# Performance work log

Hardware: AMD Instinct MI355X
Metric: run time of the kernel (lower is better)

The kernel has to match this reference:

```python
import jax, jax.numpy as jnp
import numpy as np

B, CIN, COUT, H, W = 2, 64, 64, 64, 2048
EPS = 1e-5


def unfold3(x):
    # x: [B, C, H, W] -> [B, H*W, 9, C], torch.nn.Unfold(k=3, pad=1) layout
    b, c, h, w = x.shape
    xp = jnp.pad(x, ((0, 0), (0, 0), (1, 1), (1, 1)))
    # kernel positions in row-major (ki, kj) order; index 4 is the center
    patches = jnp.stack([xp[:, :, i:i + h, j:j + w]
                         for i in range(3) for j in range(3)], axis=2)  # [B,C,9,H,W]
    return patches.reshape(b, c, 9, h * w).transpose(0, 3, 2, 1)  # [B,HW,9,C]


def setup_inputs() -> dict:
    key = jax.random.key(0)
    ks = jax.random.split(key, 8)
    x = jax.random.normal(ks[0], (B, 3 + CIN, H, W), dtype=jnp.float32)
    mask = jax.random.randint(ks[1], (B, 1, H, W), 0, 2, dtype=jnp.int32)
    w_spatial = jax.random.normal(ks[2], (CIN, 4), dtype=jnp.float32) * 0.5
    b_spatial = jax.random.normal(ks[3], (CIN,), dtype=jnp.float32) * 0.1
    w_channel = jax.random.normal(ks[4], (CIN, 4), dtype=jnp.float32) * 0.5
    b_channel = jax.random.normal(ks[5], (CIN,), dtype=jnp.float32) * 0.1
    w_agg = jax.random.normal(ks[6], (COUT, 9 * CIN), dtype=jnp.float32) * (1.0 / np.sqrt(9 * CIN))
    gamma = jnp.ones((COUT,), dtype=jnp.float32)
    beta = jnp.zeros((COUT,), dtype=jnp.float32)
    return {"x": x, "mask": mask, "w_spatial": w_spatial, "b_spatial": b_spatial,
            "w_channel": w_channel, "b_channel": b_channel, "w_agg": w_agg,
            "gamma": gamma, "beta": beta}


def reference(x, mask, w_spatial, b_spatial, w_channel, b_channel, w_agg, gamma, beta):
    b, _, h, w = x.shape
    x_un = unfold3(x)                              # [B,HW,9,3+C]
    feat = x_un[..., 3:]                           # [B,HW,9,C]
    x_pn = x_un[..., :3]                           # [B,HW,9,3]
    m_un = unfold3(mask.astype(jnp.float32))       # [B,HW,9,1]

    rng = jnp.linalg.norm(x_pn, axis=-1, keepdims=True)
    x_pn4 = jnp.concatenate([x_pn, rng], axis=-1)  # [B,HW,9,4]
    pn_p0 = x_pn4 - x_pn4[:, :, 4:5, :]            # relative to 3x3 center

    ws = jnp.einsum('bnkm,cm->bnkc', pn_p0, w_spatial) + b_spatial
    wc = jnp.einsum('bnkm,cm->bnkc', pn_p0, w_channel) + b_channel
    ws = jnp.max(ws, axis=3, keepdims=True)        # [B,HW,9,1]
    wc = jnp.max(wc, axis=2, keepdims=True)        # [B,HW,1,C]
    ws = jax.nn.softmax(ws, axis=2)
    wc = jax.nn.softmax(wc, axis=3)
    weights = (ws + wc) * m_un                     # [B,HW,9,C]

    feat = (weights * feat).reshape(b, h * w, 9 * CIN)
    out = jnp.einsum('bnf,of->bno', feat, w_agg)   # [B,HW,COUT]
    out = out.transpose(0, 2, 1)                   # [B,COUT,HW]

    # BatchNorm1d in training mode: stats over (batch, spatial) per channel
    mu = jnp.mean(out, axis=(0, 2), keepdims=True)
    var = jnp.mean((out - mu) ** 2, axis=(0, 2), keepdims=True)
    out = (out - mu) * jax.lax.rsqrt(var + EPS)
    out = out * gamma[None, :, None] + beta[None, :, None]
    out = jax.nn.relu(out)
    return out.reshape(b, COUT, h, w)              # Fold(k=1) == reshape
```

## Files before the change

### kernel.cpp

```cpp
#include <hip/hip_runtime.h>
#include <hip/hip_bf16.h>
#include <math.h>
#include <cstddef>

#define HDIM 64
#define WDIM 2048
#define HW   (HDIM*WDIM)
#define BATCH 2
#define CIN  64
#define COUT 64
#define XC   (3+CIN)
#define NPIX (BATCH*HW)
#define NBLK (NPIX/64)
#define NB2  (NBLK*2)
#define EPS  1e-5f

typedef short  short8  __attribute__((ext_vector_type(8)));
typedef float  f32x16  __attribute__((ext_vector_type(16)));

__device__ __forceinline__ unsigned short f2bf(float f) {
    unsigned int u = __float_as_uint(f);
    u += 0x7fff + ((u >> 16) & 1);
    return (unsigned short)(u >> 16);
}

struct __align__(16) SmemA {
    float wsm[9][64];
    float wcpart[4][64];
    float wcsum[4][64];
    float wc[64][64];
    union {
        unsigned short V[2][64][72];
        float wspart[9][4][64];
    } u;
};

__global__ __launch_bounds__(256)
void kernelW(const float* __restrict__ w_agg, unsigned short* __restrict__ wbf)
{
    int t = blockIdx.x*256 + threadIdx.x;
    int co  = t / 72;
    int rem = t % 72;
    int kk  = rem >> 3;
    int ks  = (rem >> 1) & 3;
    int half= rem & 1;
    const float* src = w_agg + (size_t)co*576 + kk*64 + ks*16 + half*8;
    unsigned long long pk0 = 0, pk1 = 0;
    #pragma unroll
    for (int j=0;j<4;++j) pk0 |= (unsigned long long)f2bf(src[j])   << (16*j);
    #pragma unroll
    for (int j=0;j<4;++j) pk1 |= (unsigned long long)f2bf(src[4+j]) << (16*j);
    unsigned long long* dst =
        (unsigned long long*)(wbf + ((size_t)(((kk*4+ks)*2+half)*64 + co))*8);
    dst[0] = pk0; dst[1] = pk1;
}

__global__ __launch_bounds__(256, 4)
void kernelA(const float* __restrict__ x, const int* __restrict__ mask,
             const float* __restrict__ w_sp, const float* __restrict__ b_sp,
             const float* __restrict__ w_ch, const float* __restrict__ b_ch,
             const unsigned short* __restrict__ wbf,
             float* __restrict__ out, float* __restrict__ psum, float* __restrict__ psq)
{
    __shared__ SmemA s;
    const int tid = threadIdx.x;
    const int bid = blockIdx.x;
    const int b  = bid >> 11;
    const int r  = bid & 2047;
    const int h  = r >> 5;
    const int w0 = (r & 31) << 6;

    const int px = tid & 63;
    const int q  = tid >> 6;

    float p[9][4];
    float mkr[9];
    {
        const int wpix = w0 + px;
        #pragma unroll
        for (int k = 0; k < 9; ++k) {
            int hh = h + k/3 - 1;
            int ww = wpix + k%3 - 1;
            bool in = (hh >= 0) && (hh < HDIM) && (ww >= 0) && (ww < WDIM);
            float p0=0.f, p1=0.f, p2=0.f, mv=0.f;
            if (in) {
                size_t base = ((size_t)(b*XC)*HDIM + hh)*(size_t)WDIM + ww;
                p0 = x[base];
                p1 = x[base + (size_t)HW];
                p2 = x[base + 2*(size_t)HW];
                mv = (float)mask[((size_t)b*HDIM + hh)*(size_t)WDIM + ww];
            }
            p[k][0]=p0; p[k][1]=p1; p[k][2]=p2;
            p[k][3]=sqrtf(p0*p0 + p1*p1 + p2*p2);
            mkr[k]=mv;
        }
        float c0=p[4][0], c1=p[4][1], c2=p[4][2], c3=p[4][3];
        #pragma unroll
        for (int k = 0; k < 9; ++k) {
            p[k][0]-=c0; p[k][1]-=c1; p[k][2]-=c2; p[k][3]-=c3;
        }
    }

    float wsp[9];
    #pragma unroll
    for (int k=0;k<9;++k) wsp[k] = -1e30f;
    float tmaxv[16];
    float cqm = -1e30f;
    for (int cc = 0; cc < 16; ++cc) {
        int c = q*16 + cc;
        float a0=w_sp[c*4+0], a1=w_sp[c*4+1], a2=w_sp[c*4+2], a3=w_sp[c*4+3], bs=b_sp[c];
        float d0=w_ch[c*4+0], d1=w_ch[c*4+1], d2=w_ch[c*4+2], d3=w_ch[c*4+3], bc=b_ch[c];
        float tmax = bc;
        wsp[4] = fmaxf(wsp[4], bs);
        #pragma unroll
        for (int k=0;k<9;++k) {
            if (k == 4) continue;
            float sv = fmaf(p[k][0],a0, fmaf(p[k][1],a1, fmaf(p[k][2],a2, fmaf(p[k][3],a3, bs))));
            wsp[k] = fmaxf(wsp[k], sv);
            float tv = fmaf(p[k][0],d0, fmaf(p[k][1],d1, fmaf(p[k][2],d2, fmaf(p[k][3],d3, bc))));
            tmax = fmaxf(tmax, tv);
        }
        tmaxv[cc] = tmax;
        cqm = fmaxf(cqm, tmax);
    }
    #pragma unroll
    for (int k=0;k<9;++k) s.u.wspart[k][q][px] = wsp[k];
    s.wcpart[q][px] = cqm;
    __syncthreads();

    {
        float mxc = fmaxf(fmaxf(s.wcpart[0][px], s.wcpart[1][px]),
                          fmaxf(s.wcpart[2][px], s.wcpart[3][px]));
        float sum = 0.f;
        #pragma unroll
        for (int cc=0; cc<16; ++cc) {
            float e = __expf(tmaxv[cc] - mxc);
            s.wc[q*16+cc][px] = e;
            sum += e;
        }
        s.wcsum[q][px] = sum;
    }
    if (q == 0) {
        float v[9]; float mx = -1e30f;
        #pragma unroll
        for (int k=0;k<9;++k) {
            float a = s.u.wspart[k][0][px];
            a = fmaxf(a, s.u.wspart[k][1][px]);
            a = fmaxf(a, s.u.wspart[k][2][px]);
            a = fmaxf(a, s.u.wspart[k][3][px]);
            v[k]=a; mx=fmaxf(mx,a);
        }
        float sum=0.f;
        #pragma unroll
        for (int k=0;k<9;++k) { v[k]=__expf(v[k]-mx); sum+=v[k]; }
        float inv = 1.0f/sum;
        #pragma unroll
        for (int k=0;k<9;++k) s.wsm[k][px] = v[k]*inv*mkr[k];
    }
    __syncthreads();

    const float winv = 1.0f / (s.wcsum[0][px] + s.wcsum[1][px] +
                               s.wcsum[2][px] + s.wcsum[3][px]);

    const int lane = tid & 63;
    const int wv   = tid >> 6;
    const int mrow = lane & 31;
    const int half = lane >> 5;
    const int co0  = (wv & 1) * 32;
    const int px0  = (wv >> 1) * 32;

    const short8* aswz = (const short8*)wbf;

    f32x16 acc;
    #pragma unroll
    for (int i=0;i<16;++i) acc[i]=0.f;

    auto stage_load = [&](int kk, float* f) {
        int di = kk/3 - 1, dj = (kk%3) - 1;
        int hh = h + di;
        int ww = w0 + px + dj;
        bool inb = (hh>=0) && (hh<HDIM) && (ww>=0) && (ww<WDIM);
        int hhc = hh<0?0:(hh>HDIM-1?HDIM-1:hh);
        int wwc = ww<0?0:(ww>WDIM-1?WDIM-1:ww);
        const float* xb = x + ((size_t)(b*XC + 3)*HDIM + hhc)*(size_t)WDIM + wwc;
        #pragma unroll
        for (int j=0;j<16;++j)
            f[j] = inb ? xb[(size_t)(16*q + j)*HW] : 0.f;
    };
    auto stage_write = [&](int kk, const float* f, int buf) {
        float a_k = s.wsm[kk][px];
        float m2  = mkr[kk] * winv;
        unsigned int packed[8];
        #pragma unroll
        for (int j=0;j<8;++j) {
            unsigned c0 = 16u*q + 2u*j;
            float w0f = fmaf(m2, s.wc[c0][px],   a_k) * f[2*j];
            float w1f = fmaf(m2, s.wc[c0+1][px], a_k) * f[2*j+1];
            __hip_bfloat162 h2 = __float22bfloat162_rn(float2{w0f, w1f});
            unsigned int u; __builtin_memcpy(&u, &h2, 4);
            packed[j] = u;
        }
        uint4* vp = (uint4*)&s.u.V[buf][px][16*q];
        vp[0] = uint4{packed[0],packed[1],packed[2],packed[3]};
        vp[1] = uint4{packed[4],packed[5],packed[6],packed[7]};
    };

    {
        float f0[16];
        stage_load(0, f0);
        stage_write(0, f0, 0);
        __syncthreads();
    }

    for (int kk = 0; kk < 9; ++kk) {
        short8 afc[4];
        #pragma unroll
        for (int ks=0; ks<4; ++ks)
            afc[ks] = aswz[(size_t)(((kk*4+ks)*2+half)*64) + co0 + mrow];

        float fn[16];
        if (kk < 8) stage_load(kk+1, fn);

        const unsigned short* Vb = &s.u.V[kk & 1][px0 + mrow][0];
        #pragma unroll
        for (int ks=0; ks<4; ++ks) {
            short8 bf = *(const short8*)&Vb[ks*16 + half*8];
            acc = __builtin_amdgcn_mfma_f32_32x32x16_bf16(afc[ks], bf, acc, 0, 0, 0);
        }

        if (kk < 8) {
            stage_write(kk+1, fn, (kk & 1) ^ 1);
            __syncthreads();
        }
    }

    const int pxg = w0 + px0 + mrow;
    #pragma unroll
    for (int reg=0; reg<16; ++reg) {
        int row = (reg&3) + 8*(reg>>2) + 4*half;
        int co  = co0 + row;
        float v = acc[reg];
        out[((size_t)(b*COUT+co))*HW + (size_t)h*WDIM + pxg] = v;
        float s1 = v, s2 = v*v;
        #pragma unroll
        for (int m=1; m<32; m<<=1) {
            s1 += __shfl_xor(s1, m, 64);
            s2 += __shfl_xor(s2, m, 64);
        }
        if (mrow == 0) {
            psum[(size_t)co*NB2 + bid*2 + (wv>>1)] = s1;
            psq [(size_t)co*NB2 + bid*2 + (wv>>1)] = s2;
        }
    }
}

__global__ __launch_bounds__(256)
void kernelB(const float* __restrict__ psum, const float* __restrict__ psq,
             float* __restrict__ stats)
{
    int co = blockIdx.x;
    int tid = threadIdx.x;
    float s=0.f, sq=0.f;
    for (int j = tid; j < NB2; j += 256) {
        s  += psum[(size_t)co*NB2 + j];
        sq += psq [(size_t)co*NB2 + j];
    }
    #pragma unroll
    for (int m=1; m<64; m<<=1) { s += __shfl_xor(s,m,64); sq += __shfl_xor(sq,m,64); }
    __shared__ float rs[4], rq[4];
    int wv = tid>>6;
    if ((tid&63)==0){ rs[wv]=s; rq[wv]=sq; }
    __syncthreads();
    if (tid==0) {
        float S = rs[0]+rs[1]+rs[2]+rs[3];
        float Q = rq[0]+rq[1]+rq[2]+rq[3];
        float mu = S / (float)NPIX;
        float var = Q/(float)NPIX - mu*mu;
        stats[co]      = mu;
        stats[64+co]   = rsqrtf(var + EPS);
    }
}

__global__ __launch_bounds__(256)
void kernelC(float* __restrict__ out, const float* __restrict__ stats,
             const float* __restrict__ gamma, const float* __restrict__ beta)
{
    size_t idx8 = (size_t)blockIdx.x*256 + threadIdx.x;
    size_t flat = idx8*8;
    int co = (int)((flat >> 17) & 63);
    float mu = stats[co], rstd = stats[64+co];
    float g  = gamma[co]*rstd;
    float bb = fmaf(-mu, g, beta[co]);
    #pragma unroll
    for (int t=0;t<2;++t) {
        float4 v = *(float4*)(out + flat + t*4);
        v.x = fmaxf(fmaf(v.x, g, bb), 0.f);
        v.y = fmaxf(fmaf(v.y, g, bb), 0.f);
        v.z = fmaxf(fmaf(v.z, g, bb), 0.f);
        v.w = fmaxf(fmaf(v.w, g, bb), 0.f);
        *(float4*)(out + flat + t*4) = v;
    }
}

extern "C" void kernel_launch(void* const* d_in, const int* in_sizes, int n_in,
                              void* d_out, int out_size, void* d_ws, size_t ws_size,
                              hipStream_t stream)
{
    const float* x     = (const float*)d_in[0];
    const int*   mask  = (const int*)  d_in[1];
    const float* w_sp  = (const float*)d_in[2];
    const float* b_sp  = (const float*)d_in[3];
    const float* w_ch  = (const float*)d_in[4];
    const float* b_ch  = (const float*)d_in[5];
    const float* w_agg = (const float*)d_in[6];
    const float* gamma = (const float*)d_in[7];
    const float* beta  = (const float*)d_in[8];
    float* out  = (float*)d_out;
    float* psum = (float*)d_ws;
    float* psq  = psum + (size_t)COUT*NB2;
    float* stats= psq  + (size_t)COUT*NB2;
    unsigned short* wbf = (unsigned short*)(stats + 128);

    kernelW<<<18, 256, 0, stream>>>(w_agg, wbf);
    kernelA<<<NBLK, 256, 0, stream>>>(x, mask, w_sp, b_sp, w_ch, b_ch, wbf, out, psum, psq);
    kernelB<<<COUT, 256, 0, stream>>>(psum, psq, stats);
    int grid_c = (NPIX*COUT/8)/256;
    kernelC<<<grid_c, 256, 0, stream>>>(out, stats, gamma, beta);
}
```

Measured before the change: 290.3 us.

## Stage 3-row halo feature tile in LDS once and build weighted operand in registers

Instead of reloading all 64 channels from global memory for each of the 9 kernel offsets, the block loads a 3x66 halo tile of bf16 features into swizzled LDS once. The per-channel softmax exponentials are also stored as bf16 in LDS, with per-quarter max rescaling. Each MFMA B fragment is then formed in registers from the feature and exp values, so the per-offset barriers and double-buffered staging go away. This cuts redundant global reads (about 9x reuse) and synchronisation, at the cost of extra ALU work in the MMA loop, more LDS, and bf16 rounding of the inputs before weighting.

```diff
diff --git a/kernel.cpp b/kernel.cpp
--- a/kernel.cpp
+++ b/kernel.cpp
@@ -26,11 +26,12 @@
 
 struct __align__(16) SmemA {
     float wsm[9][64];
+    float mk9[9][64];
     float wcpart[4][64];
     float wcsum[4][64];
-    float wc[64][64];
+    unsigned short E[4096];
     union {
-        unsigned short V[2][64][72];
+        unsigned short feat[12672];
         float wspart[9][4][64];
     } u;
 };
@@ -104,7 +105,7 @@
     float wsp[9];
     #pragma unroll
     for (int k=0;k<9;++k) wsp[k] = -1e30f;
-    float tmaxv[16];
+    float wclog[16];
     float cqm = -1e30f;
     for (int cc = 0; cc < 16; ++cc) {
         int c = q*16 + cc;
@@ -120,7 +121,7 @@
             float tv = fmaf(p[k][0],d0, fmaf(p[k][1],d1, fmaf(p[k][2],d2, fmaf(p[k][3],d3, bc))));
             tmax = fmaxf(tmax, tv);
         }
-        tmaxv[cc] = tmax;
+        wclog[cc] = tmax;
         cqm = fmaxf(cqm, tmax);
     }
     #pragma unroll
@@ -129,15 +130,9 @@
     __syncthreads();
 
     {
-        float mxc = fmaxf(fmaxf(s.wcpart[0][px], s.wcpart[1][px]),
-                          fmaxf(s.wcpart[2][px], s.wcpart[3][px]));
         float sum = 0.f;
         #pragma unroll
-        for (int cc=0; cc<16; ++cc) {
-            float e = __expf(tmaxv[cc] - mxc);
-            s.wc[q*16+cc][px] = e;
-            sum += e;
-        }
+        for (int cc=0; cc<16; ++cc) sum += __expf(wclog[cc] - cqm);
         s.wcsum[q][px] = sum;
     }
     if (q == 0) {
@@ -155,12 +150,63 @@
         for (int k=0;k<9;++k) { v[k]=__expf(v[k]-mx); sum+=v[k]; }
         float inv = 1.0f/sum;
         #pragma unroll
-        for (int k=0;k<9;++k) s.wsm[k][px] = v[k]*inv*mkr[k];
-    }
-    __syncthreads();
-
-    const float winv = 1.0f / (s.wcsum[0][px] + s.wcsum[1][px] +
-                               s.wcsum[2][px] + s.wcsum[3][px]);
+        for (int k=0;k<9;++k) {
+            s.wsm[k][px] = v[k]*inv*mkr[k];
+            s.mk9[k][px] = mkr[k];
+        }
+    }
+    __syncthreads();
+
+    {
+        for (int i = 0; i < 24; ++i) {
+            int task = q*24 + i;
+            int row  = task >> 5;
+            int c0   = (task & 31) * 2;
+            int hh   = h + row - 1;
+            bool rowOK = (hh >= 0) && (hh < HDIM);
+            int hhc = rowOK ? hh : 0;
+            const float* xb = x + ((size_t)(b*XC + 3 + c0)*HDIM + hhc)*(size_t)WDIM;
+            float v0 = rowOK ? xb[w0 + px]             : 0.f;
+            float v1 = rowOK ? xb[(size_t)HW + w0 + px]: 0.f;
+            unsigned int u = (unsigned int)f2bf(v0) | ((unsigned int)f2bf(v1) << 16);
+            int idx = ((row*66 + px + 1)*64 + c0) ^ (((px+1)&7)<<3);
+            *(unsigned int*)&s.u.feat[idx] = u;
+            if (px < 2) {
+                int pxi = (px==0) ? 0 : 65;
+                int ww  = (px==0) ? (w0-1) : (w0+64);
+                bool ok = rowOK && (ww >= 0) && (ww < WDIM);
+                float e0 = ok ? xb[ww]             : 0.f;
+                float e1 = ok ? xb[(size_t)HW + ww]: 0.f;
+                unsigned int ue = (unsigned int)f2bf(e0) | ((unsigned int)f2bf(e1) << 16);
+                int idxe = ((row*66 + pxi)*64 + c0) ^ ((pxi&7)<<3);
+                *(unsigned int*)&s.u.feat[idxe] = ue;
+            }
+        }
+    }
+    __syncthreads();
+
+    {
+        float M = fmaxf(fmaxf(s.wcpart[0][px], s.wcpart[1][px]),
+                        fmaxf(s.wcpart[2][px], s.wcpart[3][px]));
+        #pragma unroll
+        for (int j=0; j<8; ++j) {
+            float e0 = __expf(wclog[2*j]   - M);
+            float e1 = __expf(wclog[2*j+1] - M);
+            unsigned int u = (unsigned int)f2bf(e0) | ((unsigned int)f2bf(e1) << 16);
+            int idx = (px*64 + q*16 + 2*j) ^ ((px&7)<<3);
+            *(unsigned int*)&s.E[idx] = u;
+        }
+        if (q == 0) {
+            float tot = 0.f;
+            #pragma unroll
+            for (int jw=0; jw<4; ++jw)
+                tot += s.wcsum[jw][px] * __expf(s.wcpart[jw][px] - M);
+            float winv = 1.0f / tot;
+            #pragma unroll
+            for (int k=0;k<9;++k) s.mk9[k][px] *= winv;
+        }
+    }
+    __syncthreads();
 
     const int lane = tid & 63;
     const int wv   = tid >> 6;
@@ -168,77 +214,58 @@
     const int half = lane >> 5;
     const int co0  = (wv & 1) * 32;
     const int px0  = (wv >> 1) * 32;
+    const int pxB  = px0 + mrow;
 
     const short8* aswz = (const short8*)wbf;
+    const int ebase = pxB*64;
+    const int swze  = (pxB & 7) << 3;
 
     f32x16 acc;
     #pragma unroll
     for (int i=0;i<16;++i) acc[i]=0.f;
 
-    auto stage_load = [&](int kk, float* f) {
-        int di = kk/3 - 1, dj = (kk%3) - 1;
-        int hh = h + di;
-        int ww = w0 + px + dj;
-        bool inb = (hh>=0) && (hh<HDIM) && (ww>=0) && (ww<WDIM);
-        int hhc = hh<0?0:(hh>HDIM-1?HDIM-1:hh);
-        int wwc = ww<0?0:(ww>WDIM-1?WDIM-1:ww);
-        const float* xb = x + ((size_t)(b*XC + 3)*HDIM + hhc)*(size_t)WDIM + wwc;
-        #pragma unroll
-        for (int j=0;j<16;++j)
-            f[j] = inb ? xb[(size_t)(16*q + j)*HW] : 0.f;
-    };
-    auto stage_write = [&](int kk, const float* f, int buf) {
-        float a_k = s.wsm[kk][px];
-        float m2  = mkr[kk] * winv;
-        unsigned int packed[8];
-        #pragma unroll
-        for (int j=0;j<8;++j) {
-            unsigned c0 = 16u*q + 2u*j;
-            float w0f = fmaf(m2, s.wc[c0][px],   a_k) * f[2*j];
-            float w1f = fmaf(m2, s.wc[c0+1][px], a_k) * f[2*j+1];
-            __hip_bfloat162 h2 = __float22bfloat162_rn(float2{w0f, w1f});
-            unsigned int u; __builtin_memcpy(&u, &h2, 4);
-            packed[j] = u;
-        }
-        uint4* vp = (uint4*)&s.u.V[buf][px][16*q];
-        vp[0] = uint4{packed[0],packed[1],packed[2],packed[3]};
-        vp[1] = uint4{packed[4],packed[5],packed[6],packed[7]};
-    };
-
-    {
-        float f0[16];
-        stage_load(0, f0);
-        stage_write(0, f0, 0);
-        __syncthreads();
-    }
-
     for (int kk = 0; kk < 9; ++kk) {
+        const int row = kk/3;
+        const int dj  = kk%3 - 1;
+        const int pxi = pxB + dj + 1;
+        const int fbase = (row*66 + pxi)*64;
+        const int swzf  = (pxi & 7) << 3;
+        const float a_k = s.wsm[kk][pxB];
+        const float m2  = s.mk9[kk][pxB];
+
         short8 afc[4];
         #pragma unroll
         for (int ks=0; ks<4; ++ks)
             afc[ks] = aswz[(size_t)(((kk*4+ks)*2+half)*64) + co0 + mrow];
 
-        float fn[16];
-        if (kk < 8) stage_load(kk+1, fn);
-
-        const unsigned short* Vb = &s.u.V[kk & 1][px0 + mrow][0];
         #pragma unroll
         for (int ks=0; ks<4; ++ks) {
-            short8 bf = *(const short8*)&Vb[ks*16 + half*8];
-            acc = __builtin_amdgcn_mfma_f32_32x32x16_bf16(afc[ks], bf, acc, 0, 0, 0);
-        }
-
-        if (kk < 8) {
-            stage_write(kk+1, fn, (kk & 1) ^ 1);
-            __syncthreads();
+            const int coff = ks*16 + half*8;
+            union { short8 v; unsigned int u[4]; } fd, ed;
+            fd.v = *(const short8*)&s.u.feat[(fbase + coff) ^ swzf];
+            ed.v = *(const short8*)&s.E[(ebase + coff) ^ swze];
+            unsigned int outp[4];
+            #pragma unroll
+            for (int j=0;j<4;++j) {
+                float f0 = __uint_as_float(fd.u[j] << 16);
+                float f1 = __uint_as_float(fd.u[j] & 0xffff0000u);
+                float e0 = __uint_as_float(ed.u[j] << 16);
+                float e1 = __uint_as_float(ed.u[j] & 0xffff0000u);
+                float v0 = fmaf(m2, e0, a_k) * f0;
+                float v1 = fmaf(m2, e1, a_k) * f1;
+                __hip_bfloat162 h2 = __float22bfloat162_rn(float2{v0, v1});
+                __builtin_memcpy(&outp[j], &h2, 4);
+            }
+            short8 bfr; __builtin_memcpy(&bfr, outp, 16);
+            acc = __builtin_amdgcn_mfma_f32_32x32x16_bf16(afc[ks], bfr, acc, 0, 0, 0);
         }
     }
 
     const int pxg = w0 + px0 + mrow;
     #pragma unroll
     for (int reg=0; reg<16; ++reg) {
-        int row = (reg&3) + 8*(reg>>2) + 4*half;
-        int co  = co0 + row;
+        int rrow = (reg&3) + 8*(reg>>2) + 4*half;
+        int co   = co0 + rrow;
         float v = acc[reg];
         out[((size_t)(b*COUT+co))*HW + (size_t)h*WDIM + pxg] = v;
         float s1 = v, s2 = v*v;
```

After: 323.0 us. 1.11x slower.
